# Performance work log

Measured on AMD Instinct MI355X. Metric: run time of the kernel, lower is better.

Reference implementation:

```python
import jax, jax.numpy as jnp
import numpy as np

N = 200_000          # active voxels
C = 64               # in/out channels
K = 3                # kernel size per dim
SHAPE = (128, 128, 128)  # spatial grid (D, H, W)
B = 2                # batch size
KV = K ** 3          # 27 kernel offsets


def setup_inputs() -> dict:
    key = jax.random.key(0)
    kb, kz, ky, kx, kf, k0, k1 = jax.random.split(key, 7)
    b = jax.random.randint(kb, (N, 1), 0, B, dtype=jnp.int32)
    z = jax.random.randint(kz, (N, 1), 0, SHAPE[0], dtype=jnp.int32)
    y = jax.random.randint(ky, (N, 1), 0, SHAPE[1], dtype=jnp.int32)
    x = jax.random.randint(kx, (N, 1), 0, SHAPE[2], dtype=jnp.int32)
    coors = jnp.concatenate([b, z, y, x], axis=1)  # [N, 4] (batch, z, y, x)
    features = jax.random.normal(kf, (N, C), dtype=jnp.float32)
    W0 = jax.random.normal(k0, (KV, C, C), dtype=jnp.float32) * 0.05  # layer 0 weights per offset
    W1 = jax.random.normal(k1, (KV, C, C), dtype=jnp.float32) * 0.05  # layer 1 weights per offset
    return {"features": features, "coors": coors, "W0": W0, "W1": W1, "batch_size": B}


def _neighbor_indices(coors, batch_size):
    """Rulebook: for each of the 27 kernel offsets, index of the active input
    voxel feeding each active output voxel, or -1 if that neighbor is inactive."""
    D, H, W = SHAPE
    n = coors.shape[0]
    # dense coord -> row-index hash grid
    flat = ((coors[:, 0] * D + coors[:, 1]) * H + coors[:, 2]) * W + coors[:, 3]
    grid = jnp.full((batch_size * D * H * W,), -1, dtype=jnp.int32)
    grid = grid.at[flat].set(jnp.arange(n, dtype=jnp.int32))
    r = K // 2
    ax = jnp.arange(-r, r + 1, dtype=jnp.int32)
    offs = jnp.stack(jnp.meshgrid(ax, ax, ax, indexing="ij"), axis=-1).reshape(-1, 3)  # [27, 3]
    shp = jnp.array(SHAPE, dtype=jnp.int32)
    nb_coord = coors[None, :, 1:] + offs[:, None, :]               # [27, N, 3]
    valid = jnp.all((nb_coord >= 0) & (nb_coord < shp), axis=-1)   # [27, N]
    nc = jnp.clip(nb_coord, 0, shp - 1)
    nflat = ((coors[None, :, 0] * D + nc[..., 0]) * H + nc[..., 1]) * W + nc[..., 2]
    nb = grid[nflat]                                               # [27, N]
    return jnp.where(valid, nb, -1)


def _subm_conv(feats, W, nb):
    # gather -> per-offset GEMM -> accumulate (all offsets fused in one einsum)
    mask = (nb >= 0)
    g = feats[jnp.maximum(nb, 0)] * mask[..., None].astype(feats.dtype)  # [27, N, C]
    return jnp.einsum("knc,kco->no", g, W)  # [N, C]


def reference(features, coors, W0, W1, batch_size):
    coors = coors.astype(jnp.int32)
    nb = _neighbor_indices(coors, batch_size)  # active set is preserved across subm layers
    x = _subm_conv(features, W0, nb)
    return _subm_conv(x, W1, nb)
```

## Files before the change

kernel.cpp:

```cpp
#include <hip/hip_runtime.h>
#include <stdint.h>

#define SD 128
#define SH 128
#define SW 128
#define BATCH 2
#define CCH 64
#define KV 27
#define NCELL (BATCH * SD * SH * SW)
#define CHUNK 4096
#define NCHUNK (NCELL / CHUNK)

typedef __attribute__((ext_vector_type(4))) float f32x4;
typedef __attribute__((ext_vector_type(8))) short s16x8;

__device__ __forceinline__ unsigned short f2bf_rne(float f) {
    union { float f; unsigned int u; } v; v.f = f;
    unsigned int u = v.u;
    return (unsigned short)((u + 0x7FFFu + ((u >> 16) & 1u)) >> 16);
}

__device__ __forceinline__ s16x8 pack_bf8(float4 a, float4 b) {
    s16x8 o;
    o[0] = (short)f2bf_rne(a.x); o[1] = (short)f2bf_rne(a.y);
    o[2] = (short)f2bf_rne(a.z); o[3] = (short)f2bf_rne(a.w);
    o[4] = (short)f2bf_rne(b.x); o[5] = (short)f2bf_rne(b.y);
    o[6] = (short)f2bf_rne(b.z); o[7] = (short)f2bf_rne(b.w);
    return o;
}


__global__ void k_wprep(const float* __restrict__ W, unsigned short* __restrict__ Wt) {
    int idx = blockIdx.x * blockDim.x + threadIdx.x;
    if (idx >= KV * CCH * CCH) return;
    int k = idx / (CCH * CCH);
    int rem = idx - k * CCH * CCH;
    int ci = rem >> 6, co = rem & 63;
    int d = ((k * 8 + (ci >> 3)) * 64 + co) * 8 + (ci & 7);
    Wt[d] = f2bf_rne(W[idx]);
}

__global__ void k_scatter(const int4* __restrict__ coors, int* __restrict__ grid, int n) {
    int i = blockIdx.x * blockDim.x + threadIdx.x;
    if (i >= n) return;
    int4 c = coors[i];
    int flat = ((c.x * SD + c.y) * SH + c.z) * SW + c.w;
    atomicMax(&grid[flat], i);
}


__global__ void k_count(const int4* __restrict__ grid4, int* __restrict__ counts) {
    int t = threadIdx.x;
    size_t base = (size_t)blockIdx.x * (CHUNK / 4) + t * 4;
    int cnt = 0;
#pragma unroll
    for (int i = 0; i < 4; ++i) {
        int4 v = grid4[base + i];
        cnt += (v.x >= 0) + (v.y >= 0) + (v.z >= 0) + (v.w >= 0);
    }
    __shared__ int s[256];
    s[t] = cnt; __syncthreads();
    for (int d = 128; d > 0; d >>= 1) {
        if (t < d) s[t] += s[t + d];
        __syncthreads();
    }
    if (t == 0) counts[blockIdx.x] = s[0];
}

__global__ void k_scan(const int* __restrict__ counts, int* __restrict__ excl, int* __restrict__ ctr) {
    __shared__ int s[NCHUNK];
    int t = threadIdx.x;
    int v = counts[t];
    s[t] = v; __syncthreads();
    for (int d = 1; d < NCHUNK; d <<= 1) {
        int a = (t >= d) ? s[t - d] : 0;
        __syncthreads();
        s[t] += a;
        __syncthreads();
    }
    excl[t] = s[t] - v;
    if (t == NCHUNK - 1) ctr[0] = s[t];
}

__global__ void k_compact(int* __restrict__ grid, const int* __restrict__ excl,
                          int* __restrict__ perm) {
    int t = threadIdx.x;
    size_t cellbase = (size_t)blockIdx.x * CHUNK + t * 16;
    int v[16];
    const int4* g4 = (const int4*)(grid + cellbase);
#pragma unroll
    for (int i = 0; i < 4; ++i) {
        int4 a = g4[i];
        v[i * 4 + 0] = a.x; v[i * 4 + 1] = a.y; v[i * 4 + 2] = a.z; v[i * 4 + 3] = a.w;
    }
    int cnt = 0;
#pragma unroll
    for (int i = 0; i < 16; ++i) cnt += (v[i] >= 0);
    __shared__ int s[256];
    s[t] = cnt; __syncthreads();
    for (int d = 1; d < 256; d <<= 1) {
        int a = (t >= d) ? s[t - d] : 0;
        __syncthreads();
        s[t] += a;
        __syncthreads();
    }
    int idx = excl[blockIdx.x] + s[t] - cnt;
#pragma unroll
    for (int i = 0; i < 16; ++i) {
        if (v[i] >= 0) {
            perm[idx] = v[i];
            grid[cellbase + i] = idx;
            idx++;
        }
    }
}

__global__ void k_losers(const int4* __restrict__ coors, const int* __restrict__ grid,
                         int* __restrict__ perm, int* __restrict__ ctr, int n) {
    int j = blockIdx.x * blockDim.x + threadIdx.x;
    if (j >= n) return;
    int4 c = coors[j];
    int flat = ((c.x * SD + c.y) * SH + c.z) * SW + c.w;
    int si = grid[flat];
    if (perm[si] != j) {
        int s = atomicAdd(ctr, 1);
        perm[s] = j;
    }
}

__global__ void k_permfeat(const float4* __restrict__ feats4, const int4* __restrict__ coors,
                           const int* __restrict__ perm, s16x8* __restrict__ fs,
                           int* __restrict__ fb, int n) {
    int tid = blockIdx.x * blockDim.x + threadIdx.x;
    int i = tid >> 3, j = tid & 7;
    if (i >= n) return;
    int src = perm[i];
    float4 p0 = feats4[(size_t)src * 16 + j * 2];
    float4 p1 = feats4[(size_t)src * 16 + j * 2 + 1];
    fs[(size_t)i * 8 + j] = pack_bf8(p0, p1);
    if (j == 0) {
        int4 c = coors[src];
        fb[i] = ((c.x * SD + c.y) * SH + c.z) * SW + c.w;
    }
}

template <int OUT_PERM>
__global__ __launch_bounds__(256) void k_conv_s(const s16x8* __restrict__ fin,
                                                const s16x8* __restrict__ wt,
                                                const int* __restrict__ fb,
                                                const int* __restrict__ grid,
                                                const int* __restrict__ perm,
                                                void* __restrict__ outp, int n) {
    int nwg = gridDim.x, orig = blockIdx.x;
    int q = nwg >> 3, rr = nwg & 7;
    int xcd = orig & 7, bidx = orig >> 3;
    int blk = (xcd < rr ? xcd * (q + 1) : rr * (q + 1) + (xcd - rr) * q) + bidx;

    int wid = blk * (blockDim.x >> 6) + (threadIdx.x >> 6);
    int lane = threadIdx.x & 63;
    int base = wid * 32;
    if (base >= n) return;
    int r = lane & 15;
    int g = lane >> 4;
    int li = lane & 31;
    int myrow = base + li;
    int rowok = (myrow < n) ? 1 : 0;
    int fbv = fb[rowok ? myrow : 0];
    int pl = 0;
    if (OUT_PERM) pl = rowok ? perm[myrow] : 0;
    int z = (fbv >> 14) & 127, y = (fbv >> 7) & 127, x = fbv & 127;

    f32x4 acc[2][4] = {};

    auto lookup = [&](int k) -> int {
        int dz = k / 9 - 1, dy = (k / 3) % 3 - 1, dx = k % 3 - 1;
        int zz = z + dz, yy = y + dy, xx = x + dx;
        int v = -1;
        if (rowok && (unsigned)zz < SD && (unsigned)yy < SH && (unsigned)xx < SW)
            v = grid[fbv + dz * (SH * SW) + dy * SW + dx];
        return v;
    };

    int nbr = lookup(0);
    for (int k = 0; k < KV; ++k) {
        int nbr_next = (k + 1 < KV) ? lookup(k + 1) : -1;
        int nb0 = __shfl(nbr, r);
        int nb1 = __shfl(nbr, 16 + r);
        nbr = nbr_next;
        unsigned long long m0 = __ballot(nb0 >= 0);
        unsigned long long m1 = __ballot(nb1 >= 0);
        if ((m0 | m1) == 0ULL) continue;

        s16x8 bf[2][4];
#pragma unroll
        for (int s = 0; s < 2; ++s)
#pragma unroll
            for (int t = 0; t < 4; ++t)
                bf[s][t] = wt[(k * 8 + s * 4 + g) * 64 + t * 16 + r];

        int nbh[2] = {nb0, nb1};
        unsigned long long mm[2] = {m0, m1};
#pragma unroll
        for (int h = 0; h < 2; ++h) {
            if (!mm[h]) continue;
            int nbx = nbh[h];
            s16x8 a0 = {}, a1 = {};
            if (nbx >= 0) {
                a0 = fin[(size_t)nbx * 8 + g];
                a1 = fin[(size_t)nbx * 8 + 4 + g];
            }
#pragma unroll
            for (int t = 0; t < 4; ++t) {
                acc[h][t] = __builtin_amdgcn_mfma_f32_16x16x32_bf16(a0, bf[0][t], acc[h][t], 0, 0, 0);
                acc[h][t] = __builtin_amdgcn_mfma_f32_16x16x32_bf16(a1, bf[1][t], acc[h][t], 0, 0, 0);
            }
        }
    }

    if (OUT_PERM) {
        float* __restrict__ o = (float*)outp;
#pragma unroll
        for (int h = 0; h < 2; ++h)
#pragma unroll
            for (int t = 0; t < 4; ++t)
#pragma unroll
                for (int j = 0; j < 4; ++j) {
                    int w = h * 16 + g * 4 + j;
                    if (base + w < n) {
                        int orow = __shfl(pl, w);
                        o[(size_t)orow * 64 + t * 16 + r] = acc[h][t][j];
                    }
                }
    } else {
        unsigned short* __restrict__ o = (unsigned short*)outp;
#pragma unroll
        for (int h = 0; h < 2; ++h)
#pragma unroll
            for (int t = 0; t < 4; ++t)
#pragma unroll
                for (int j = 0; j < 4; ++j) {
                    int row = base + h * 16 + g * 4 + j;
                    if (row < n) o[(size_t)row * 64 + t * 16 + r] = f2bf_rne(acc[h][t][j]);
                }
    }
}


__global__ void k_f2bf(const float4* __restrict__ in, ushort4* __restrict__ out, int n4) {
    int i = blockIdx.x * blockDim.x + threadIdx.x;
    if (i >= n4) return;
    float4 a = in[i];
    ushort4 o;
    o.x = f2bf_rne(a.x); o.y = f2bf_rne(a.y);
    o.z = f2bf_rne(a.z); o.w = f2bf_rne(a.w);
    out[i] = o;
}

template <int IN_F32, int OUT_BF16>
__global__ __launch_bounds__(256) void k_conv_legacy(const void* __restrict__ finv,
                                                     const s16x8* __restrict__ wt,
                                                     const int4* __restrict__ coors,
                                                     const int* __restrict__ grid,
                                                     void* __restrict__ outp, int n) {
    int wid = blockIdx.x * (blockDim.x >> 6) + (threadIdx.x >> 6);
    int lane = threadIdx.x & 63;
    int base = wid * 32;
    if (base >= n) return;
    int r = lane & 15;
    int g = lane >> 4;
    int li = lane & 31;
    int myrow = base + li;
    int rowok = (myrow < n) ? 1 : 0;
    int4 c = coors[rowok ? myrow : 0];
    int z = c.y, y = c.z, x = c.w;
    int flatbase = ((c.x * SD + z) * SH + y) * SW + x;

    f32x4 acc[2][4] = {};

    auto lookup = [&](int k) -> int {
        int dz = k / 9 - 1, dy = (k / 3) % 3 - 1, dx = k % 3 - 1;
        int zz = z + dz, yy = y + dy, xx = x + dx;
        int v = -1;
        if (rowok && (unsigned)zz < SD && (unsigned)yy < SH && (unsigned)xx < SW)
            v = grid[flatbase + dz * (SH * SW) + dy * SW + dx];
        return v;
    };

    int nbr = lookup(0);
    for (int k = 0; k < KV; ++k) {
        int nbr_next = (k + 1 < KV) ? lookup(k + 1) : -1;
        int nb0 = __shfl(nbr, r);
        int nb1 = __shfl(nbr, 16 + r);
        nbr = nbr_next;
        unsigned long long m0 = __ballot(nb0 >= 0);
        unsigned long long m1 = __ballot(nb1 >= 0);
        if ((m0 | m1) == 0ULL) continue;

        s16x8 bf[2][4];
#pragma unroll
        for (int s = 0; s < 2; ++s)
#pragma unroll
            for (int t = 0; t < 4; ++t)
                bf[s][t] = wt[(k * 8 + s * 4 + g) * 64 + t * 16 + r];

        int nbh[2] = {nb0, nb1};
        unsigned long long mm[2] = {m0, m1};
#pragma unroll
        for (int h = 0; h < 2; ++h) {
            if (!mm[h]) continue;
            int nbx = nbh[h];
            s16x8 a0 = {}, a1 = {};
            if (nbx >= 0) {
                if (IN_F32) {
                    const float4* ff = (const float4*)finv;
                    size_t rb = (size_t)nbx * 16 + g * 2;
                    float4 p0 = ff[rb], p1 = ff[rb + 1];
                    float4 p2 = ff[rb + 8], p3 = ff[rb + 9];
                    a0 = pack_bf8(p0, p1);
                    a1 = pack_bf8(p2, p3);
                } else {
                    const s16x8* fbp = (const s16x8*)finv;
                    a0 = fbp[(size_t)nbx * 8 + g];
                    a1 = fbp[(size_t)nbx * 8 + 4 + g];
                }
            }
#pragma unroll
            for (int t = 0; t < 4; ++t) {
                acc[h][t] = __builtin_amdgcn_mfma_f32_16x16x32_bf16(a0, bf[0][t], acc[h][t], 0, 0, 0);
                acc[h][t] = __builtin_amdgcn_mfma_f32_16x16x32_bf16(a1, bf[1][t], acc[h][t], 0, 0, 0);
            }
        }
    }

    if (OUT_BF16) {
        unsigned short* __restrict__ o = (unsigned short*)outp;
#pragma unroll
        for (int h = 0; h < 2; ++h)
#pragma unroll
            for (int t = 0; t < 4; ++t)
#pragma unroll
                for (int j = 0; j < 4; ++j) {
                    int row = base + h * 16 + g * 4 + j;
                    if (row < n) o[(size_t)row * 64 + t * 16 + r] = f2bf_rne(acc[h][t][j]);
                }
    } else {
        float* __restrict__ o = (float*)outp;
#pragma unroll
        for (int h = 0; h < 2; ++h)
#pragma unroll
            for (int t = 0; t < 4; ++t)
#pragma unroll
                for (int j = 0; j < 4; ++j) {
                    int row = base + h * 16 + g * 4 + j;
                    if (row < n) o[(size_t)row * 64 + t * 16 + r] = acc[h][t][j];
                }
    }
}

extern "C" void kernel_launch(void* const* d_in, const int* in_sizes, int n_in,
                              void* d_out, int out_size, void* d_ws, size_t ws_size,
                              hipStream_t stream) {
    const float* feats = (const float*)d_in[0];
    const int4* coors = (const int4*)d_in[1];
    const float* W0 = (const float*)d_in[2];
    const float* W1 = (const float*)d_in[3];
    int N = in_sizes[0] / CCH;

    char* p0 = (char*)d_ws;
    char* p = p0;
    auto carve = [&](size_t bytes) -> char* {
        char* q = p;
        p += (bytes + 255) & ~(size_t)255;
        return q;
    };

    size_t grid_bytes = (size_t)NCELL * 4;
    int* grid = (int*)carve(grid_bytes);
    unsigned short* wt0 = (unsigned short*)carve((size_t)KV * CCH * CCH * 2);
    unsigned short* wt1 = (unsigned short*)carve((size_t)KV * CCH * CCH * 2);

    char* psave = p;
    int* counts = (int*)carve(NCHUNK * 4);
    int* excl = (int*)carve(NCHUNK * 4);
    int* ctr = (int*)carve(256);
    int* perm = (int*)carve((size_t)N * 4);
    int* fb = (int*)carve((size_t)N * 4);
    s16x8* fs = (s16x8*)carve((size_t)N * CCH * 2);
    s16x8* ibf_s = (s16x8*)carve((size_t)N * CCH * 2);
    bool sorted_ok = (size_t)(p - p0) <= ws_size;

    int nw = KV * CCH * CCH;
    int tiles = (N + 31) / 32;
    int blocks = (tiles + 3) / 4;

    hipMemsetAsync(grid, 0xFF, grid_bytes, stream);
    k_wprep<<<(nw + 255) / 256, 256, 0, stream>>>(W0, wt0);
    k_wprep<<<(nw + 255) / 256, 256, 0, stream>>>(W1, wt1);
    k_scatter<<<(N + 255) / 256, 256, 0, stream>>>(coors, grid, N);

    if (sorted_ok) {
        k_count<<<NCHUNK, 256, 0, stream>>>((const int4*)grid, counts);
        k_scan<<<1, NCHUNK, 0, stream>>>(counts, excl, ctr);
        k_compact<<<NCHUNK, 256, 0, stream>>>(grid, excl, perm);
        k_losers<<<(N + 255) / 256, 256, 0, stream>>>(coors, grid, perm, ctr, N);
        k_permfeat<<<((N * 8) + 255) / 256, 256, 0, stream>>>((const float4*)feats, coors, perm, fs, fb, N);
        k_conv_s<0><<<blocks, 256, 0, stream>>>(fs, (const s16x8*)wt0, fb, grid, perm, ibf_s, N);
        k_conv_s<1><<<blocks, 256, 0, stream>>>(ibf_s, (const s16x8*)wt1, fb, grid, perm, d_out, N);
    } else {
        p = psave;
        s16x8* ibf = (s16x8*)carve((size_t)N * CCH * 2);
        size_t base_need = (size_t)(p - p0);
        s16x8* fbf = nullptr;
        if (ws_size >= base_need + (size_t)N * CCH * 2 + 256)
            fbf = (s16x8*)carve((size_t)N * CCH * 2);
        if (fbf) {
            int n4 = N * CCH / 4;
            k_f2bf<<<(n4 + 255) / 256, 256, 0, stream>>>((const float4*)feats, (ushort4*)fbf, n4);
            k_conv_legacy<0, 1><<<blocks, 256, 0, stream>>>(fbf, (const s16x8*)wt0, coors, grid, ibf, N);
        } else {
            k_conv_legacy<1, 1><<<blocks, 256, 0, stream>>>(feats, (const s16x8*)wt0, coors, grid, ibf, N);
        }
        k_conv_legacy<0, 0><<<blocks, 256, 0, stream>>>(ibf, (const s16x8*)wt1, coors, grid, d_out, N);
    }
}
```

Baseline: 318.7 us.

## Stage conv weights in double-buffered LDS and use warp-shuffle scan

The sparse conv kernel now stages each kernel offset's 64x64 bf16 weight slice in double-buffered shared memory. The next offset's slice is prefetched into registers while the current one is consumed, and a block barrier follows every offset. This replaces per-wave global weight loads with LDS reads shared by the four waves in a block. The cost is one __syncthreads per offset, and all waves must run the loop, so the early exit was removed. The single-block scan is rewritten as a wave-shuffle scan with a small cross-wave pass, and the legacy fallback path and its kernels are deleted.

```diff
diff --git a/kernel.cpp b/kernel.cpp
--- a/kernel.cpp
+++ b/kernel.cpp
@@ -68,18 +68,30 @@
 }
 
 __global__ void k_scan(const int* __restrict__ counts, int* __restrict__ excl, int* __restrict__ ctr) {
-    __shared__ int s[NCHUNK];
-    int t = threadIdx.x;
+    int t = threadIdx.x, lane = t & 63, w = t >> 6;
     int v = counts[t];
-    s[t] = v; __syncthreads();
-    for (int d = 1; d < NCHUNK; d <<= 1) {
-        int a = (t >= d) ? s[t - d] : 0;
-        __syncthreads();
-        s[t] += a;
-        __syncthreads();
-    }
-    excl[t] = s[t] - v;
-    if (t == NCHUNK - 1) ctr[0] = s[t];
+    int s = v;
+#pragma unroll
+    for (int d = 1; d < 64; d <<= 1) {
+        int u = __shfl_up(s, d);
+        if (lane >= d) s += u;
+    }
+    __shared__ int wsum[16];
+    if (lane == 63) wsum[w] = s;
+    __syncthreads();
+    if (w == 0 && lane < 16) {
+        int x = wsum[lane];
+#pragma unroll
+        for (int d = 1; d < 16; d <<= 1) {
+            int u = __shfl_up(x, d);
+            if (lane >= d) x += u;
+        }
+        wsum[lane] = x;
+    }
+    __syncthreads();
+    int add = (w > 0) ? wsum[w - 1] : 0;
+    excl[t] = add + s - v;
+    if (t == 1023) ctr[0] = add + s;
 }
 
 __global__ void k_compact(int* __restrict__ grid, const int* __restrict__ excl,
@@ -151,15 +163,17 @@
                                                 const int* __restrict__ grid,
                                                 const int* __restrict__ perm,
                                                 void* __restrict__ outp, int n) {
+    __shared__ s16x8 wbuf[2][512];
+
     int nwg = gridDim.x, orig = blockIdx.x;
     int q = nwg >> 3, rr = nwg & 7;
     int xcd = orig & 7, bidx = orig >> 3;
     int blk = (xcd < rr ? xcd * (q + 1) : rr * (q + 1) + (xcd - rr) * q) + bidx;
 
-    int wid = blk * (blockDim.x >> 6) + (threadIdx.x >> 6);
-    int lane = threadIdx.x & 63;
+    int tid = threadIdx.x;
+    int w = tid >> 6, lane = tid & 63;
+    int wid = blk * 4 + w;
     int base = wid * 32;
-    if (base >= n) return;
     int r = lane & 15;
     int g = lane >> 4;
     int li = lane & 31;
@@ -181,40 +195,58 @@
         return v;
     };
 
+    {
+        s16x8 s0 = wt[tid];
+        s16x8 s1 = wt[256 + tid];
+        wbuf[0][tid] = s0;
+        wbuf[0][256 + tid] = s1;
+    }
+    __syncthreads();
+
     int nbr = lookup(0);
     for (int k = 0; k < KV; ++k) {
+        int kn = (k + 1 < KV) ? k + 1 : KV - 1;
+        s16x8 st0 = wt[(size_t)kn * 512 + tid];
+        s16x8 st1 = wt[(size_t)kn * 512 + 256 + tid];
+
         int nbr_next = (k + 1 < KV) ? lookup(k + 1) : -1;
         int nb0 = __shfl(nbr, r);
         int nb1 = __shfl(nbr, 16 + r);
         nbr = nbr_next;
         unsigned long long m0 = __ballot(nb0 >= 0);
         unsigned long long m1 = __ballot(nb1 >= 0);
-        if ((m0 | m1) == 0ULL) continue;
-
-        s16x8 bf[2][4];
-#pragma unroll
-        for (int s = 0; s < 2; ++s)
-#pragma unroll
-            for (int t = 0; t < 4; ++t)
-                bf[s][t] = wt[(k * 8 + s * 4 + g) * 64 + t * 16 + r];
-
-        int nbh[2] = {nb0, nb1};
-        unsigned long long mm[2] = {m0, m1};
-#pragma unroll
-        for (int h = 0; h < 2; ++h) {
-            if (!mm[h]) continue;
-            int nbx = nbh[h];
-            s16x8 a0 = {}, a1 = {};
-            if (nbx >= 0) {
-                a0 = fin[(size_t)nbx * 8 + g];
-                a1 = fin[(size_t)nbx * 8 + 4 + g];
-            }
-#pragma unroll
-            for (int t = 0; t < 4; ++t) {
-                acc[h][t] = __builtin_amdgcn_mfma_f32_16x16x32_bf16(a0, bf[0][t], acc[h][t], 0, 0, 0);
-                acc[h][t] = __builtin_amdgcn_mfma_f32_16x16x32_bf16(a1, bf[1][t], acc[h][t], 0, 0, 0);
+
+        if (m0 | m1) {
+            const s16x8* wb = &wbuf[k & 1][0];
+            s16x8 bf[2][4];
+#pragma unroll
+            for (int s = 0; s < 2; ++s)
+#pragma unroll
+                for (int t = 0; t < 4; ++t)
+                    bf[s][t] = wb[(s * 4 + g) * 64 + t * 16 + r];
+
+            int nbh[2] = {nb0, nb1};
+            unsigned long long mm[2] = {m0, m1};
+#pragma unroll
+            for (int h = 0; h < 2; ++h) {
+                if (!mm[h]) continue;
+                int nbx = nbh[h];
+                s16x8 a0 = {}, a1 = {};
+                if (nbx >= 0) {
+                    a0 = fin[(size_t)nbx * 8 + g];
+                    a1 = fin[(size_t)nbx * 8 + 4 + g];
+                }
+#pragma unroll
+                for (int t = 0; t < 4; ++t) {
+                    acc[h][t] = __builtin_amdgcn_mfma_f32_16x16x32_bf16(a0, bf[0][t], acc[h][t], 0, 0, 0);
+                    acc[h][t] = __builtin_amdgcn_mfma_f32_16x16x32_bf16(a1, bf[1][t], acc[h][t], 0, 0, 0);
+                }
             }
         }
+
+        wbuf[(k + 1) & 1][tid] = st0;
+        wbuf[(k + 1) & 1][256 + tid] = st1;
+        __syncthreads();
     }
 
     if (OUT_PERM) {
@@ -225,9 +257,9 @@
             for (int t = 0; t < 4; ++t)
 #pragma unroll
                 for (int j = 0; j < 4; ++j) {
-                    int w = h * 16 + g * 4 + j;
-                    if (base + w < n) {
-                        int orow = __shfl(pl, w);
+                    int ww = h * 16 + g * 4 + j;
+                    if (base + ww < n) {
+                        int orow = __shfl(pl, ww);
                         o[(size_t)orow * 64 + t * 16 + r] = acc[h][t][j];
                     }
                 }
@@ -241,118 +273,6 @@
                 for (int j = 0; j < 4; ++j) {
                     int row = base + h * 16 + g * 4 + j;
                     if (row < n) o[(size_t)row * 64 + t * 16 + r] = f2bf_rne(acc[h][t][j]);
-                }
-    }
-}
-
-
-__global__ void k_f2bf(const float4* __restrict__ in, ushort4* __restrict__ out, int n4) {
-    int i = blockIdx.x * blockDim.x + threadIdx.x;
-    if (i >= n4) return;
-    float4 a = in[i];
-    ushort4 o;
-    o.x = f2bf_rne(a.x); o.y = f2bf_rne(a.y);
-    o.z = f2bf_rne(a.z); o.w = f2bf_rne(a.w);
-    out[i] = o;
-}
-
-template <int IN_F32, int OUT_BF16>
-__global__ __launch_bounds__(256) void k_conv_legacy(const void* __restrict__ finv,
-                                                     const s16x8* __restrict__ wt,
-                                                     const int4* __restrict__ coors,
-                                                     const int* __restrict__ grid,
-                                                     void* __restrict__ outp, int n) {
-    int wid = blockIdx.x * (blockDim.x >> 6) + (threadIdx.x >> 6);
-    int lane = threadIdx.x & 63;
-    int base = wid * 32;
-    if (base >= n) return;
-    int r = lane & 15;
-    int g = lane >> 4;
-    int li = lane & 31;
-    int myrow = base + li;
-    int rowok = (myrow < n) ? 1 : 0;
-    int4 c = coors[rowok ? myrow : 0];
-    int z = c.y, y = c.z, x = c.w;
-    int flatbase = ((c.x * SD + z) * SH + y) * SW + x;
-
-    f32x4 acc[2][4] = {};
-
-    auto lookup = [&](int k) -> int {
-        int dz = k / 9 - 1, dy = (k / 3) % 3 - 1, dx = k % 3 - 1;
-        int zz = z + dz, yy = y + dy, xx = x + dx;
-        int v = -1;
-        if (rowok && (unsigned)zz < SD && (unsigned)yy < SH && (unsigned)xx < SW)
-            v = grid[flatbase + dz * (SH * SW) + dy * SW + dx];
-        return v;
-    };
-
-    int nbr = lookup(0);
-    for (int k = 0; k < KV; ++k) {
-        int nbr_next = (k + 1 < KV) ? lookup(k + 1) : -1;
-        int nb0 = __shfl(nbr, r);
-        int nb1 = __shfl(nbr, 16 + r);
-        nbr = nbr_next;
-        unsigned long long m0 = __ballot(nb0 >= 0);
-        unsigned long long m1 = __ballot(nb1 >= 0);
-        if ((m0 | m1) == 0ULL) continue;
-
-        s16x8 bf[2][4];
-#pragma unroll
-        for (int s = 0; s < 2; ++s)
-#pragma unroll
-            for (int t = 0; t < 4; ++t)
-                bf[s][t] = wt[(k * 8 + s * 4 + g) * 64 + t * 16 + r];
-
-        int nbh[2] = {nb0, nb1};
-        unsigned long long mm[2] = {m0, m1};
-#pragma unroll
-        for (int h = 0; h < 2; ++h) {
-            if (!mm[h]) continue;
-            int nbx = nbh[h];
-            s16x8 a0 = {}, a1 = {};
-            if (nbx >= 0) {
-                if (IN_F32) {
-                    const float4* ff = (const float4*)finv;
-                    size_t rb = (size_t)nbx * 16 + g * 2;
-                    float4 p0 = ff[rb], p1 = ff[rb + 1];
-                    float4 p2 = ff[rb + 8], p3 = ff[rb + 9];
-                    a0 = pack_bf8(p0, p1);
-                    a1 = pack_bf8(p2, p3);
-                } else {
-                    const s16x8* fbp = (const s16x8*)finv;
-                    a0 = fbp[(size_t)nbx * 8 + g];
-                    a1 = fbp[(size_t)nbx * 8 + 4 + g];
-                }
-            }
-#pragma unroll
-            for (int t = 0; t < 4; ++t) {
-                acc[h][t] = __builtin_amdgcn_mfma_f32_16x16x32_bf16(a0, bf[0][t], acc[h][t], 0, 0, 0);
-                acc[h][t] = __builtin_amdgcn_mfma_f32_16x16x32_bf16(a1, bf[1][t], acc[h][t], 0, 0, 0);
-            }
-        }
-    }
-
-    if (OUT_BF16) {
-        unsigned short* __restrict__ o = (unsigned short*)outp;
-#pragma unroll
-        for (int h = 0; h < 2; ++h)
-#pragma unroll
-            for (int t = 0; t < 4; ++t)
-#pragma unroll
-                for (int j = 0; j < 4; ++j) {
-                    int row = base + h * 16 + g * 4 + j;
-                    if (row < n) o[(size_t)row * 64 + t * 16 + r] = f2bf_rne(acc[h][t][j]);
-                }
-    } else {
-        float* __restrict__ o = (float*)outp;
-#pragma unroll
-        for (int h = 0; h < 2; ++h)
-#pragma unroll
-            for (int t = 0; t < 4; ++t)
-#pragma unroll
-                for (int j = 0; j < 4; ++j) {
-                    int row = base + h * 16 + g * 4 + j;
-                    if (row < n) o[(size_t)row * 64 + t * 16 + r] = acc[h][t][j];
                 }
     }
 }
@@ -366,8 +286,7 @@
     const float* W1 = (const float*)d_in[3];
     int N = in_sizes[0] / CCH;
 
-    char* p0 = (char*)d_ws;
-    char* p = p0;
+    char* p = (char*)d_ws;
     auto carve = [&](size_t bytes) -> char* {
         char* q = p;
         p += (bytes + 255) & ~(size_t)255;
@@ -378,8 +297,6 @@
     int* grid = (int*)carve(grid_bytes);
     unsigned short* wt0 = (unsigned short*)carve((size_t)KV * CCH * CCH * 2);
     unsigned short* wt1 = (unsigned short*)carve((size_t)KV * CCH * CCH * 2);
-
-    char* psave = p;
     int* counts = (int*)carve(NCHUNK * 4);
     int* excl = (int*)carve(NCHUNK * 4);
     int* ctr = (int*)carve(256);
@@ -387,7 +304,6 @@
     int* fb = (int*)carve((size_t)N * 4);
     s16x8* fs = (s16x8*)carve((size_t)N * CCH * 2);
     s16x8* ibf_s = (s16x8*)carve((size_t)N * CCH * 2);
-    bool sorted_ok = (size_t)(p - p0) <= ws_size;
 
     int nw = KV * CCH * CCH;
     int tiles = (N + 31) / 32;
@@ -397,29 +313,11 @@
     k_wprep<<<(nw + 255) / 256, 256, 0, stream>>>(W0, wt0);
     k_wprep<<<(nw + 255) / 256, 256, 0, stream>>>(W1, wt1);
     k_scatter<<<(N + 255) / 256, 256, 0, stream>>>(coors, grid, N);
-
-    if (sorted_ok) {
-        k_count<<<NCHUNK, 256, 0, stream>>>((const int4*)grid, counts);
-        k_scan<<<1, NCHUNK, 0, stream>>>(counts, excl, ctr);
-        k_compact<<<NCHUNK, 256, 0, stream>>>(grid, excl, perm);
-        k_losers<<<(N + 255) / 256, 256, 0, stream>>>(coors, grid, perm, ctr, N);
-        k_permfeat<<<((N * 8) + 255) / 256, 256, 0, stream>>>((const float4*)feats, coors, perm, fs, fb, N);
-        k_conv_s<0><<<blocks, 256, 0, stream>>>(fs, (const s16x8*)wt0, fb, grid, perm, ibf_s, N);
-        k_conv_s<1><<<blocks, 256, 0, stream>>>(ibf_s, (const s16x8*)wt1, fb, grid, perm, d_out, N);
-    } else {
-        p = psave;
-        s16x8* ibf = (s16x8*)carve((size_t)N * CCH * 2);
-        size_t base_need = (size_t)(p - p0);
-        s16x8* fbf = nullptr;
-        if (ws_size >= base_need + (size_t)N * CCH * 2 + 256)
-            fbf = (s16x8*)carve((size_t)N * CCH * 2);
-        if (fbf) {
-            int n4 = N * CCH / 4;
-            k_f2bf<<<(n4 + 255) / 256, 256, 0, stream>>>((const float4*)feats, (ushort4*)fbf, n4);
-            k_conv_legacy<0, 1><<<blocks, 256, 0, stream>>>(fbf, (const s16x8*)wt0, coors, grid, ibf, N);
-        } else {
-            k_conv_legacy<1, 1><<<blocks, 256, 0, stream>>>(feats, (const s16x8*)wt0, coors, grid, ibf, N);
-        }
-        k_conv_legacy<0, 0><<<blocks, 256, 0, stream>>>(ibf, (const s16x8*)wt1, coors, grid, d_out, N);
-    }
-}
+    k_count<<<NCHUNK, 256, 0, stream>>>((const int4*)grid, counts);
+    k_scan<<<1, 1024, 0, stream>>>(counts, excl, ctr);
+    k_compact<<<NCHUNK, 256, 0, stream>>>(grid, excl, perm);
+    k_losers<<<(N + 255) / 256, 256, 0, stream>>>(coors, grid, perm, ctr, N);
+    k_permfeat<<<((N * 8) + 255) / 256, 256, 0, stream>>>((const float4*)feats, coors, perm, fs, fb, N);
+    k_conv_s<0><<<blocks, 256, 0, stream>>>(fs, (const s16x8*)wt0, fb, grid, perm, ibf_s, N);
+    k_conv_s<1><<<blocks, 256, 0, stream>>>(ibf_s, (const s16x8*)wt1, fb, grid, perm, d_out, N);
+}
```

Result: faster. 298.8 us (-6.2%).
